# Optimization experiments

Hardware: AMD Instinct MI355X
Metric: run time of the kernel (lower is better)

Reference implementation:

```python
import jax, jax.numpy as jnp
import numpy as np

B, S, D, NH = 1024, 128, 512, 8
DH = D // NH  # head dim = 64


def setup_inputs() -> dict:
    key = jax.random.key(0)
    ks = jax.random.split(key, 9)
    scale = 1.0 / np.sqrt(D)
    return {
        "x_non": jax.random.normal(ks[0], (B, D), jnp.float32),
        "x_seq": jax.random.normal(ks[1], (B, S, D), jnp.float32),
        "mask": jax.random.randint(ks[2], (B, NH, S), 0, 2, jnp.int32),
        "Wq": jax.random.normal(ks[3], (D, D), jnp.float32) * scale,
        "bq": jax.random.normal(ks[4], (D,), jnp.float32) * scale,
        "Wk": jax.random.normal(ks[5], (D, D), jnp.float32) * scale,
        "bk": jax.random.normal(ks[6], (D,), jnp.float32) * scale,
        "Wv": jax.random.normal(ks[7], (D, D), jnp.float32) * scale,
        "bv": jax.random.normal(ks[8], (D,), jnp.float32) * scale,
    }


def reference(x_non, x_seq, mask, Wq, bq, Wk, bk, Wv, bv):
    batch, seq_len, dim = x_seq.shape
    nhead = NH
    dh = dim // nhead
    # Linear projections (torch Linear: y = x @ W.T + b)
    q = (x_non @ Wq.T + bq).reshape(batch, nhead, dh)           # (b, n, d)
    k = (x_seq @ Wk.T + bk).reshape(batch, seq_len, nhead, dh)  # (b, s, n, d)
    v = (x_seq @ Wv.T + bv).reshape(batch, seq_len, nhead, dh)
    qk = jnp.einsum("bnd,bsnd->bns", q, k)
    # NOTE: source uses `//` (floor division) by sqrt(d_head) -- reproduced faithfully
    qk = jnp.floor(qk / jnp.sqrt(jnp.asarray(dh, qk.dtype)))
    qk = jnp.where(mask == 0, jnp.asarray(-1e9, qk.dtype), qk)
    attn = jax.nn.softmax(qk, axis=-1)                           # (b, n, s)
    z = jnp.einsum("bns,bsnd->bnd", attn, v).reshape(batch, dim)
    return z
```

## Files before the change

kernel.cpp:

```cpp
#include <hip/hip_runtime.h>

#define SS  128
#define DD  512
#define NHH 8
#define DHH 64

typedef float  f4 __attribute__((ext_vector_type(4)));
typedef float  f2 __attribute__((ext_vector_type(2)));
typedef double d2 __attribute__((ext_vector_type(2)));

typedef const void __attribute__((address_space(1)))* gas_t;
typedef void __attribute__((address_space(3)))* las_t;

__global__ __launch_bounds__(512) void qproj_kernel(
    const float* __restrict__ x_non, const float* __restrict__ Wq,
    const float* __restrict__ bq, double* __restrict__ qws)
{
    const int tid = threadIdx.x;
    const int bt  = blockIdx.x & 31;
    const int ot  = blockIdx.x >> 5;
    const int kh  = tid >> 8;
    const int t8  = tid & 255;
    const int r   = t8 >> 4, c = t8 & 15;

    __shared__ __attribute__((aligned(16))) float Xs0[32][68];
    __shared__ __attribute__((aligned(16))) float Xs1[32][68];
    __shared__ __attribute__((aligned(16))) float Ws0[64][68];
    __shared__ __attribute__((aligned(16))) float Ws1[64][68];

    double acc[2][4];
    #pragma unroll
    for (int i = 0; i < 2; ++i)
        #pragma unroll
        for (int j = 0; j < 4; ++j) acc[i][j] = 0.0;

    for (int kc = 0; kc < 4; ++kc) {
        __syncthreads();
        #pragma unroll
        for (int p = 0; p < 2; ++p) {
            int g  = tid + 512 * p;
            int rr = g >> 5, w = g & 31, hf = w >> 4, cc = (w & 15) * 4;
            f4 v = *(const f4*)(x_non + (size_t)(bt * 32 + rr) * DD + hf * 256 + kc * 64 + cc);
            if (hf) *(f4*)&Xs1[rr][cc] = v; else *(f4*)&Xs0[rr][cc] = v;
        }
        #pragma unroll
        for (int p = 0; p < 4; ++p) {
            int g  = tid + 512 * p;
            int rr = g >> 5, w = g & 31, hf = w >> 4, cc = (w & 15) * 4;
            f4 v = *(const f4*)(Wq + (size_t)(ot * 64 + rr) * DD + hf * 256 + kc * 64 + cc);
            if (hf) *(f4*)&Ws1[rr][cc] = v; else *(f4*)&Ws0[rr][cc] = v;
        }
        __syncthreads();
        const float (*Xh)[68] = kh ? Xs1 : Xs0;
        const float (*Wh)[68] = kh ? Ws1 : Ws0;
        #pragma unroll 4
        for (int kk = 0; kk < 64; ++kk) {
            double a0 = (double)Xh[r][kk];
            double a1 = (double)Xh[r + 16][kk];
            #pragma unroll
            for (int j = 0; j < 4; ++j) {
                double bb = (double)Wh[c + 16 * j][kk];
                acc[0][j] = fma(a0, bb, acc[0][j]);
                acc[1][j] = fma(a1, bb, acc[1][j]);
            }
        }
    }
    __syncthreads();
    double* S = (double*)&Ws0[0][0];
    if (kh == 1) {
        #pragma unroll
        for (int i = 0; i < 2; ++i)
            #pragma unroll
            for (int j = 0; j < 4; ++j) S[t8 * 8 + i * 4 + j] = acc[i][j];
    }
    __syncthreads();
    if (kh == 0) {
        #pragma unroll
        for (int i = 0; i < 2; ++i)
            #pragma unroll
            for (int j = 0; j < 4; ++j) {
                int o = ot * 64 + c + 16 * j;
                qws[(size_t)(bt * 32 + r + 16 * i) * DD + o] =
                    acc[i][j] + S[t8 * 8 + i * 4 + j] + (double)bq[o];
            }
    }
}

__device__ __forceinline__ void stage_chunk(const float* __restrict__ Xb,
                                            int c, int buf, int tid, float* XsF)
{
    const int wid  = tid >> 6;
    const int lane = tid & 63;
    const float* gsrc = Xb + (size_t)c * (8 * DD);
    #pragma unroll
    for (int p = 0; p < 4; ++p) {
        const int gbase = p * 256 + wid * 64;
        const float* gp = gsrc + (size_t)(gbase + lane) * 4;
        float* lp = XsF + (size_t)buf * 4096 + (size_t)gbase * 4;
        __builtin_amdgcn_global_load_lds((gas_t)gp, (las_t)lp, 16, 0, 0);
    }
}

__global__ __launch_bounds__(256) void core_kernel(
    const double* __restrict__ qws, const float* __restrict__ x_seq,
    const int* __restrict__ mask, const float* __restrict__ Wk,
    const float* __restrict__ bk, float* __restrict__ uws)
{
    const int tid = threadIdx.x;
    const int b   = blockIdx.x;
    const float* Xb = x_seq + (size_t)b * (SS * DD);

    const int hp    = tid >> 6;
    const int rhalf = (tid >> 5) & 1;
    const int k16   = tid & 31;

    __shared__ __attribute__((aligned(16))) union {
        double T[8][512];
        float  Xs[2][8][512];
    } sh;
    __shared__ __attribute__((aligned(16))) union {
        double qd[512];
        int    mk[1024];
    } sh2;
    __shared__ double qbks[8];

    float* XsF = &sh.Xs[0][0][0];

    sh2.qd[tid]       = qws[(size_t)b * DD + tid];
    sh2.qd[tid + 256] = qws[(size_t)b * DD + tid + 256];
    __syncthreads();

    if (tid < 64) {
        const int h = tid >> 3, part = tid & 7;
        double s = 0.0;
        #pragma unroll
        for (int ii = 0; ii < 8; ++ii) {
            int d = part * 8 + ii;
            s = fma(sh2.qd[h * DHH + d], (double)bk[h * DHH + d], s);
        }
        s += __shfl_xor(s, 1);
        s += __shfl_xor(s, 2);
        s += __shfl_xor(s, 4);
        if (part == 0) qbks[h] = s;
    }

    {
        const int kg = tid & 127, dh = tid >> 7;
        const int k4 = kg * 4;
        for (int hg = 0; hg < 2; ++hg) {
            double tacc[4][4];
            #pragma unroll
            for (int h4 = 0; h4 < 4; ++h4) {
                const int h = hg * 4 + h4;
                const float* wp = Wk + ((size_t)(h * DHH + dh * 32)) * DD + k4;
                double t0 = 0, t1 = 0, t2 = 0, t3 = 0;
                for (int d = 0; d < 32; ++d) {
                    f4 wv = *(const f4*)(wp + (size_t)d * DD);
                    double qv = sh2.qd[h * DHH + dh * 32 + d];
                    t0 = fma((double)wv[0], qv, t0);
                    t1 = fma((double)wv[1], qv, t1);
                    t2 = fma((double)wv[2], qv, t2);
                    t3 = fma((double)wv[3], qv, t3);
                }
                tacc[h4][0] = t0; tacc[h4][1] = t1; tacc[h4][2] = t2; tacc[h4][3] = t3;
            }
            if (dh == 1) {
                #pragma unroll
                for (int h4 = 0; h4 < 4; ++h4)
                    #pragma unroll
                    for (int e = 0; e < 4; ++e)
                        sh.T[hg * 4 + h4][k4 + e] = tacc[h4][e];
            }
            __syncthreads();
            if (dh == 0) {
                #pragma unroll
                for (int h4 = 0; h4 < 4; ++h4)
                    #pragma unroll
                    for (int e = 0; e < 4; ++e)
                        sh.T[hg * 4 + h4][k4 + e] += tacc[h4][e];
            }
            __syncthreads();
        }
    }

    d2 treg[2][8];
    #pragma unroll
    for (int hh = 0; hh < 2; ++hh)
        #pragma unroll
        for (int p = 0; p < 8; ++p)
            treg[hh][p] = *(const d2*)&sh.T[hp * 2 + hh][k16 * 2 + 64 * p];
    float qbkf[2] = { (float)qbks[hp * 2], (float)qbks[hp * 2 + 1] };
    __syncthreads();

    #pragma unroll
    for (int p = 0; p < 4; ++p)
        sh2.mk[tid + 256 * p] = mask[(size_t)b * (NHH * SS) + tid + 256 * p];
    stage_chunk(Xb, 0, 0, tid, XsF);
    asm volatile("s_waitcnt vmcnt(0)");
    __syncthreads();

    float u[2][16];
    #pragma unroll
    for (int hh = 0; hh < 2; ++hh)
        #pragma unroll
        for (int j = 0; j < 16; ++j) u[hh][j] = 0.f;
    float m_run[2] = { -1e30f, -1e30f };
    float l_run[2] = { 0.f, 0.f };

    for (int c = 0; c < 16; ++c) {
        const int buf = c & 1;
        if (c < 15) stage_chunk(Xb, c + 1, buf ^ 1, tid, XsF);

        const float* Xc = XsF + buf * 4096 + (rhalf * 4) * DD + k16 * 2;

        double acc[2][4];
        #pragma unroll
        for (int hh = 0; hh < 2; ++hh)
            #pragma unroll
            for (int r = 0; r < 4; ++r) acc[hh][r] = 0.0;

        #pragma unroll
        for (int r = 0; r < 4; ++r) {
            #pragma unroll
            for (int p = 0; p < 8; ++p) {
                f2 xv = *(const f2*)&Xc[r * DD + p * 64];
                double x0 = (double)xv[0], x1 = (double)xv[1];
                #pragma unroll
                for (int hh = 0; hh < 2; ++hh) {
                    acc[hh][r] = fma(x0, treg[hh][p][0], acc[hh][r]);
                    acc[hh][r] = fma(x1, treg[hh][p][1], acc[hh][r]);
                }
            }
        }

        float Lown[2][4];
        #pragma unroll
        for (int hh = 0; hh < 2; ++hh)
            #pragma unroll
            for (int r = 0; r < 4; ++r) {
                float s = (float)acc[hh][r];
                s += __shfl_xor(s, 1);
                s += __shfl_xor(s, 2);
                s += __shfl_xor(s, 4);
                s += __shfl_xor(s, 8);
                s += __shfl_xor(s, 16);
                s = floorf((s + qbkf[hh]) * 0.125f);
                const int row = c * 8 + rhalf * 4 + r;
                if (sh2.mk[(hp * 2 + hh) * SS + row] == 0) s = -1e9f;
                Lown[hh][r] = s;
            }

        float pw[2][4];
        #pragma unroll
        for (int hh = 0; hh < 2; ++hh) {
            float Loth[4];
            #pragma unroll
            for (int r = 0; r < 4; ++r) Loth[r] = __shfl_xor(Lown[hh][r], 32);
            float cmax = fmaxf(
                fmaxf(fmaxf(Lown[hh][0], Lown[hh][1]), fmaxf(Lown[hh][2], Lown[hh][3])),
                fmaxf(fmaxf(Loth[0], Loth[1]), fmaxf(Loth[2], Loth[3])));
            float mnew = fmaxf(m_run[hh], cmax);
            if (mnew != m_run[hh]) {
                float fs = __expf(m_run[hh] - mnew);
                #pragma unroll
                for (int j = 0; j < 16; ++j) u[hh][j] *= fs;
                l_run[hh] *= fs;
                m_run[hh] = mnew;
            }
            float ps = 0.f;
            #pragma unroll
            for (int r = 0; r < 4; ++r) { pw[hh][r] = __expf(Lown[hh][r] - mnew); ps += pw[hh][r]; }
            #pragma unroll
            for (int r = 0; r < 4; ++r) ps += __expf(Loth[r] - mnew);
            l_run[hh] += ps;
        }

        #pragma unroll
        for (int r = 0; r < 4; ++r) {
            #pragma unroll
            for (int p = 0; p < 8; ++p) {
                f2 xv = *(const f2*)&Xc[r * DD + p * 64];
                #pragma unroll
                for (int hh = 0; hh < 2; ++hh) {
                    u[hh][p * 2]     = fmaf(pw[hh][r], xv[0], u[hh][p * 2]);
                    u[hh][p * 2 + 1] = fmaf(pw[hh][r], xv[1], u[hh][p * 2 + 1]);
                }
            }
        }

        asm volatile("s_waitcnt vmcnt(0)");
        __syncthreads();
    }

    #pragma unroll
    for (int hh = 0; hh < 2; ++hh)
        #pragma unroll
        for (int j = 0; j < 16; ++j) u[hh][j] += __shfl_xor(u[hh][j], 32);

    {
        const int h = hp * 2 + rhalf;
        const float inv = 1.0f / (rhalf ? l_run[1] : l_run[0]);
        float* dst = uws + ((size_t)b * NHH + h) * DD + k16 * 2;
        #pragma unroll
        for (int p = 0; p < 8; ++p) {
            f2 v;
            v[0] = (rhalf ? u[1][p * 2]     : u[0][p * 2])     * inv;
            v[1] = (rhalf ? u[1][p * 2 + 1] : u[0][p * 2 + 1]) * inv;
            *(f2*)&dst[p * 64] = v;
        }
    }
}

__global__ __launch_bounds__(512) void zout_kernel(
    const float* __restrict__ uws, const float* __restrict__ Wv,
    const float* __restrict__ bv, float* __restrict__ out)
{
    const int tid = threadIdx.x;
    const int bt  = blockIdx.x & 31;
    const int ot  = blockIdx.x >> 5;
    const int kh  = tid >> 8;
    const int t8  = tid & 255;
    const int r   = t8 >> 4, c = t8 & 15;

    __shared__ __attribute__((aligned(16))) float Us0[32][68];
    __shared__ __attribute__((aligned(16))) float Us1[32][68];
    __shared__ __attribute__((aligned(16))) float Ws0[64][68];
    __shared__ __attribute__((aligned(16))) float Ws1[64][68];

    float acc[2][4];
    #pragma unroll
    for (int i = 0; i < 2; ++i)
        #pragma unroll
        for (int j = 0; j < 4; ++j) acc[i][j] = 0.f;

    for (int kc = 0; kc < 4; ++kc) {
        __syncthreads();
        #pragma unroll
        for (int p = 0; p < 2; ++p) {
            int g  = tid + 512 * p;
            int rr = g >> 5, w = g & 31, hf = w >> 4, cc = (w & 15) * 4;
            f4 v = *(const f4*)(uws + ((size_t)(bt * 32 + rr) * NHH + ot) * DD
                                + hf * 256 + kc * 64 + cc);
            if (hf) *(f4*)&Us1[rr][cc] = v; else *(f4*)&Us0[rr][cc] = v;
        }
        #pragma unroll
        for (int p = 0; p < 4; ++p) {
            int g  = tid + 512 * p;
            int rr = g >> 5, w = g & 31, hf = w >> 4, cc = (w & 15) * 4;
            f4 v = *(const f4*)(Wv + (size_t)(ot * 64 + rr) * DD + hf * 256 + kc * 64 + cc);
            if (hf) *(f4*)&Ws1[rr][cc] = v; else *(f4*)&Ws0[rr][cc] = v;
        }
        __syncthreads();
        const float (*Uh)[68] = kh ? Us1 : Us0;
        const float (*Wh)[68] = kh ? Ws1 : Ws0;
        #pragma unroll 4
        for (int kk = 0; kk < 64; ++kk) {
            float a0 = Uh[r][kk];
            float a1 = Uh[r + 16][kk];
            #pragma unroll
            for (int j = 0; j < 4; ++j) {
                float bb = Wh[c + 16 * j][kk];
                acc[0][j] = fmaf(a0, bb, acc[0][j]);
                acc[1][j] = fmaf(a1, bb, acc[1][j]);
            }
        }
    }
    __syncthreads();
    float* S = (float*)&Ws0[0][0];
    if (kh == 1) {
        #pragma unroll
        for (int i = 0; i < 2; ++i)
            #pragma unroll
            for (int j = 0; j < 4; ++j) S[t8 * 8 + i * 4 + j] = acc[i][j];
    }
    __syncthreads();
    if (kh == 0) {
        #pragma unroll
        for (int i = 0; i < 2; ++i)
            #pragma unroll
            for (int j = 0; j < 4; ++j) {
                int o = ot * 64 + c + 16 * j;
                out[(size_t)(bt * 32 + r + 16 * i) * DD + o] =
                    acc[i][j] + S[t8 * 8 + i * 4 + j] + bv[o];
            }
    }
}

extern "C" void kernel_launch(void* const* d_in, const int* in_sizes, int n_in,
                              void* d_out, int out_size, void* d_ws, size_t ws_size,
                              hipStream_t stream) {
    const float* x_non = (const float*)d_in[0];
    const float* x_seq = (const float*)d_in[1];
    const int*   mask  = (const int*)d_in[2];
    const float* Wq    = (const float*)d_in[3];
    const float* bq    = (const float*)d_in[4];
    const float* Wk    = (const float*)d_in[5];
    const float* bk    = (const float*)d_in[6];
    const float* Wv    = (const float*)d_in[7];
    const float* bv    = (const float*)d_in[8];
    float*       out   = (float*)d_out;

    double* qws = (double*)d_ws;
    float*  uws = (float*)((char*)d_ws + (size_t)1024 * DD * 8);

    qproj_kernel<<<256, 512, 0, stream>>>(x_non, Wq, bq, qws);
    core_kernel<<<1024, 256, 0, stream>>>(qws, x_seq, mask, Wk, bk, uws);
    zout_kernel<<<256, 512, 0, stream>>>(uws, Wv, bv, out);
}
```

Before: 480.0 us.

## Split core kernel across head groups and drop double-buffered staging

The core kernel now launches two blocks per batch row, each handling four heads with one head per wavefront, instead of one block covering all eight heads. Each thread computes its own Wk·q projection row directly in registers, with no shared-memory reduction. The double-buffered x_seq staging is replaced by a single buffer loaded synchronously each chunk. This cuts registers and LDS per block to raise occupancy and parallelism, but x_seq is read twice from global memory and load latency is no longer overlapped with compute.

```diff
diff --git a/kernel.cpp b/kernel.cpp
--- a/kernel.cpp
+++ b/kernel.cpp
@@ -87,7 +87,7 @@
 }
 
 __device__ __forceinline__ void stage_chunk(const float* __restrict__ Xb,
-                                            int c, int buf, int tid, float* XsF)
+                                            int c, int tid, float* XsF)
 {
     const int wid  = tid >> 6;
     const int lane = tid & 63;
@@ -96,7 +96,7 @@
     for (int p = 0; p < 4; ++p) {
         const int gbase = p * 256 + wid * 64;
         const float* gp = gsrc + (size_t)(gbase + lane) * 4;
-        float* lp = XsF + (size_t)buf * 4096 + (size_t)gbase * 4;
+        float* lp = XsF + (size_t)gbase * 4;
         __builtin_amdgcn_global_load_lds((gas_t)gp, (las_t)lp, 16, 0, 0);
     }
 }
@@ -106,206 +106,152 @@
     const int* __restrict__ mask, const float* __restrict__ Wk,
     const float* __restrict__ bk, float* __restrict__ uws)
 {
-    const int tid = threadIdx.x;
-    const int b   = blockIdx.x;
+    const int tid  = threadIdx.x;
+    const int b    = blockIdx.x & 1023;
+    const int hgrp = (blockIdx.x >> 10) * 4;
     const float* Xb = x_seq + (size_t)b * (SS * DD);
 
     const int hp    = tid >> 6;
+    const int h     = hgrp + hp;
     const int rhalf = (tid >> 5) & 1;
     const int k16   = tid & 31;
 
-    __shared__ __attribute__((aligned(16))) union {
-        double T[8][512];
-        float  Xs[2][8][512];
-    } sh;
+    __shared__ __attribute__((aligned(16))) float Xs[8][512];
     __shared__ __attribute__((aligned(16))) union {
         double qd[512];
         int    mk[1024];
     } sh2;
     __shared__ double qbks[8];
 
-    float* XsF = &sh.Xs[0][0][0];
-
     sh2.qd[tid]       = qws[(size_t)b * DD + tid];
     sh2.qd[tid + 256] = qws[(size_t)b * DD + tid + 256];
     __syncthreads();
 
     if (tid < 64) {
-        const int h = tid >> 3, part = tid & 7;
+        const int hh = tid >> 3, part = tid & 7;
         double s = 0.0;
         #pragma unroll
         for (int ii = 0; ii < 8; ++ii) {
             int d = part * 8 + ii;
-            s = fma(sh2.qd[h * DHH + d], (double)bk[h * DHH + d], s);
+            s = fma(sh2.qd[hh * DHH + d], (double)bk[hh * DHH + d], s);
         }
         s += __shfl_xor(s, 1);
         s += __shfl_xor(s, 2);
         s += __shfl_xor(s, 4);
-        if (part == 0) qbks[h] = s;
-    }
-
+        if (part == 0) qbks[hh] = s;
+    }
+
+    d2 treg[8];
+    #pragma unroll
+    for (int p = 0; p < 8; ++p) { treg[p][0] = 0.0; treg[p][1] = 0.0; }
     {
-        const int kg = tid & 127, dh = tid >> 7;
-        const int k4 = kg * 4;
-        for (int hg = 0; hg < 2; ++hg) {
-            double tacc[4][4];
-            #pragma unroll
-            for (int h4 = 0; h4 < 4; ++h4) {
-                const int h = hg * 4 + h4;
-                const float* wp = Wk + ((size_t)(h * DHH + dh * 32)) * DD + k4;
-                double t0 = 0, t1 = 0, t2 = 0, t3 = 0;
-                for (int d = 0; d < 32; ++d) {
-                    f4 wv = *(const f4*)(wp + (size_t)d * DD);
-                    double qv = sh2.qd[h * DHH + dh * 32 + d];
-                    t0 = fma((double)wv[0], qv, t0);
-                    t1 = fma((double)wv[1], qv, t1);
-                    t2 = fma((double)wv[2], qv, t2);
-                    t3 = fma((double)wv[3], qv, t3);
-                }
-                tacc[h4][0] = t0; tacc[h4][1] = t1; tacc[h4][2] = t2; tacc[h4][3] = t3;
-            }
-            if (dh == 1) {
-                #pragma unroll
-                for (int h4 = 0; h4 < 4; ++h4)
-                    #pragma unroll
-                    for (int e = 0; e < 4; ++e)
-                        sh.T[hg * 4 + h4][k4 + e] = tacc[h4][e];
-            }
-            __syncthreads();
-            if (dh == 0) {
-                #pragma unroll
-                for (int h4 = 0; h4 < 4; ++h4)
-                    #pragma unroll
-                    for (int e = 0; e < 4; ++e)
-                        sh.T[hg * 4 + h4][k4 + e] += tacc[h4][e];
-            }
-            __syncthreads();
-        }
-    }
-
-    d2 treg[2][8];
-    #pragma unroll
-    for (int hh = 0; hh < 2; ++hh)
-        #pragma unroll
-        for (int p = 0; p < 8; ++p)
-            treg[hh][p] = *(const d2*)&sh.T[hp * 2 + hh][k16 * 2 + 64 * p];
-    float qbkf[2] = { (float)qbks[hp * 2], (float)qbks[hp * 2 + 1] };
-    __syncthreads();
+        const float* wkh = Wk + (size_t)(h * DHH) * DD + k16 * 2;
+        for (int d = 0; d < DHH; ++d) {
+            const double qv = sh2.qd[h * DHH + d];
+            const float* wr = wkh + (size_t)d * DD;
+            #pragma unroll
+            for (int p = 0; p < 8; ++p) {
+                f2 wv = *(const f2*)(wr + p * 64);
+                treg[p][0] = fma((double)wv[0], qv, treg[p][0]);
+                treg[p][1] = fma((double)wv[1], qv, treg[p][1]);
+            }
+        }
+    }
+    __syncthreads();
+
+    const float qbkf = (float)qbks[h];
 
     #pragma unroll
     for (int p = 0; p < 4; ++p)
         sh2.mk[tid + 256 * p] = mask[(size_t)b * (NHH * SS) + tid + 256 * p];
-    stage_chunk(Xb, 0, 0, tid, XsF);
-    asm volatile("s_waitcnt vmcnt(0)");
-    __syncthreads();
-
-    float u[2][16];
-    #pragma unroll
-    for (int hh = 0; hh < 2; ++hh)
-        #pragma unroll
-        for (int j = 0; j < 16; ++j) u[hh][j] = 0.f;
-    float m_run[2] = { -1e30f, -1e30f };
-    float l_run[2] = { 0.f, 0.f };
+
+    float u[16];
+    #pragma unroll
+    for (int j = 0; j < 16; ++j) u[j] = 0.f;
+    float m_run = -1e30f;
+    float l_run = 0.f;
 
     for (int c = 0; c < 16; ++c) {
-        const int buf = c & 1;
-        if (c < 15) stage_chunk(Xb, c + 1, buf ^ 1, tid, XsF);
-
-        const float* Xc = XsF + buf * 4096 + (rhalf * 4) * DD + k16 * 2;
-
-        double acc[2][4];
-        #pragma unroll
-        for (int hh = 0; hh < 2; ++hh)
-            #pragma unroll
-            for (int r = 0; r < 4; ++r) acc[hh][r] = 0.0;
+        __syncthreads();
+        stage_chunk(Xb, c, tid, &Xs[0][0]);
+        asm volatile("s_waitcnt vmcnt(0)");
+        __syncthreads();
+
+        const float* Xc = &Xs[0][0] + (rhalf * 4) * DD + k16 * 2;
+
+        double acc[4];
+        #pragma unroll
+        for (int r = 0; r < 4; ++r) acc[r] = 0.0;
 
         #pragma unroll
         for (int r = 0; r < 4; ++r) {
             #pragma unroll
             for (int p = 0; p < 8; ++p) {
                 f2 xv = *(const f2*)&Xc[r * DD + p * 64];
-                double x0 = (double)xv[0], x1 = (double)xv[1];
-                #pragma unroll
-                for (int hh = 0; hh < 2; ++hh) {
-                    acc[hh][r] = fma(x0, treg[hh][p][0], acc[hh][r]);
-                    acc[hh][r] = fma(x1, treg[hh][p][1], acc[hh][r]);
-                }
-            }
-        }
-
-        float Lown[2][4];
-        #pragma unroll
-        for (int hh = 0; hh < 2; ++hh)
-            #pragma unroll
-            for (int r = 0; r < 4; ++r) {
-                float s = (float)acc[hh][r];
-                s += __shfl_xor(s, 1);
-                s += __shfl_xor(s, 2);
-                s += __shfl_xor(s, 4);
-                s += __shfl_xor(s, 8);
-                s += __shfl_xor(s, 16);
-                s = floorf((s + qbkf[hh]) * 0.125f);
-                const int row = c * 8 + rhalf * 4 + r;
-                if (sh2.mk[(hp * 2 + hh) * SS + row] == 0) s = -1e9f;
-                Lown[hh][r] = s;
-            }
-
-        float pw[2][4];
-        #pragma unroll
-        for (int hh = 0; hh < 2; ++hh) {
-            float Loth[4];
-            #pragma unroll
-            for (int r = 0; r < 4; ++r) Loth[r] = __shfl_xor(Lown[hh][r], 32);
-            float cmax = fmaxf(
-                fmaxf(fmaxf(Lown[hh][0], Lown[hh][1]), fmaxf(Lown[hh][2], Lown[hh][3])),
-                fmaxf(fmaxf(Loth[0], Loth[1]), fmaxf(Loth[2], Loth[3])));
-            float mnew = fmaxf(m_run[hh], cmax);
-            if (mnew != m_run[hh]) {
-                float fs = __expf(m_run[hh] - mnew);
-                #pragma unroll
-                for (int j = 0; j < 16; ++j) u[hh][j] *= fs;
-                l_run[hh] *= fs;
-                m_run[hh] = mnew;
-            }
-            float ps = 0.f;
-            #pragma unroll
-            for (int r = 0; r < 4; ++r) { pw[hh][r] = __expf(Lown[hh][r] - mnew); ps += pw[hh][r]; }
-            #pragma unroll
-            for (int r = 0; r < 4; ++r) ps += __expf(Loth[r] - mnew);
-            l_run[hh] += ps;
-        }
+                acc[r] = fma((double)xv[0], treg[p][0], acc[r]);
+                acc[r] = fma((double)xv[1], treg[p][1], acc[r]);
+            }
+        }
+
+        float Lown[4];
+        #pragma unroll
+        for (int r = 0; r < 4; ++r) {
+            float s = (float)acc[r];
+            s += __shfl_xor(s, 1);
+            s += __shfl_xor(s, 2);
+            s += __shfl_xor(s, 4);
+            s += __shfl_xor(s, 8);
+            s += __shfl_xor(s, 16);
+            s = floorf((s + qbkf) * 0.125f);
+            const int row = c * 8 + rhalf * 4 + r;
+            if (sh2.mk[h * SS + row] == 0) s = -1e9f;
+            Lown[r] = s;
+        }
+
+        float Loth[4];
+        #pragma unroll
+        for (int r = 0; r < 4; ++r) Loth[r] = __shfl_xor(Lown[r], 32);
+        float cmax = fmaxf(
+            fmaxf(fmaxf(Lown[0], Lown[1]), fmaxf(Lown[2], Lown[3])),
+            fmaxf(fmaxf(Loth[0], Loth[1]), fmaxf(Loth[2], Loth[3])));
+        float mnew = fmaxf(m_run, cmax);
+        if (mnew != m_run) {
+            float fs = __expf(m_run - mnew);
+            #pragma unroll
+            for (int j = 0; j < 16; ++j) u[j] *= fs;
+            l_run *= fs;
+            m_run = mnew;
+        }
+        float pw[4];
+        float ps = 0.f;
+        #pragma unroll
+        for (int r = 0; r < 4; ++r) { pw[r] = __expf(Lown[r] - mnew); ps += pw[r]; }
+        #pragma unroll
+        for (int r = 0; r < 4; ++r) ps += __expf(Loth[r] - mnew);
+        l_run += ps;
 
         #pragma unroll
         for (int r = 0; r < 4; ++r) {
             #pragma unroll
             for (int p = 0; p < 8; ++p) {
                 f2 xv = *(const f2*)&Xc[r * DD + p * 64];
-                #pragma unroll
-                for (int hh = 0; hh < 2; ++hh) {
-                    u[hh][p * 2]     = fmaf(pw[hh][r], xv[0], u[hh][p * 2]);
-                    u[hh][p * 2 + 1] = fmaf(pw[hh][r], xv[1], u[hh][p * 2 + 1]);
-                }
-            }
-        }
-
-        asm volatile("s_waitcnt vmcnt(0)");
-        __syncthreads();
-    }
-
-    #pragma unroll
-    for (int hh = 0; hh < 2; ++hh)
-        #pragma unroll
-        for (int j = 0; j < 16; ++j) u[hh][j] += __shfl_xor(u[hh][j], 32);
-
-    {
-        const int h = hp * 2 + rhalf;
-        const float inv = 1.0f / (rhalf ? l_run[1] : l_run[0]);
+                u[p * 2]     = fmaf(pw[r], xv[0], u[p * 2]);
+                u[p * 2 + 1] = fmaf(pw[r], xv[1], u[p * 2 + 1]);
+            }
+        }
+    }
+
+    #pragma unroll
+    for (int j = 0; j < 16; ++j) u[j] += __shfl_xor(u[j], 32);
+
+    if (rhalf == 0) {
+        const float inv = 1.0f / l_run;
         float* dst = uws + ((size_t)b * NHH + h) * DD + k16 * 2;
         #pragma unroll
         for (int p = 0; p < 8; ++p) {
             f2 v;
-            v[0] = (rhalf ? u[1][p * 2]     : u[0][p * 2])     * inv;
-            v[1] = (rhalf ? u[1][p * 2 + 1] : u[0][p * 2 + 1]) * inv;
+            v[0] = u[p * 2]     * inv;
+            v[1] = u[p * 2 + 1] * inv;
             *(f2*)&dst[p * 64] = v;
         }
     }
@@ -404,6 +350,6 @@
     float*  uws = (float*)((char*)d_ws + (size_t)1024 * DD * 8);
 
     qproj_kernel<<<256, 512, 0, stream>>>(x_non, Wq, bq, qws);
-    core_kernel<<<1024, 256, 0, stream>>>(qws, x_seq, mask, Wk, bk, uws);
+    core_kernel<<<2048, 256, 0, stream>>>(qws, x_seq, mask, Wk, bk, uws);
     zout_kernel<<<256, 512, 0, stream>>>(uws, Wv, bv, out);
 }
```

Measured after the change: 559.2 us. +16.5%, slower.
